# Kernel optimization log

Hardware: AMD Instinct MI355X
Metric: run time of the kernel (lower is better)

Reference implementation:

```python
import jax, jax.numpy as jnp
import numpy as np

D = 1024   # rnn_size
H = 64     # pooling MLP hidden
B, C = 16, 1024


def setup_inputs() -> dict:
    key = jax.random.key(0)
    ks = jax.random.split(key, 12)
    s = 1.0 / np.sqrt(D)
    inp = {
        "encoder_outputs": jax.random.normal(ks[0], (B, C, D), jnp.float32),
        # Linear weights stored as [in, out] (y = x @ W + b), same math as torch Linear
        "Wf": jax.random.uniform(ks[1], (D, D), jnp.float32, -s, s),
        "bf": jax.random.uniform(ks[2], (D,), jnp.float32, -s, s),
        "Wg": jax.random.uniform(ks[3], (D, D), jnp.float32, -s, s),
        "bg": jax.random.uniform(ks[4], (D,), jnp.float32, -s, s),
        "Wx": jax.random.uniform(ks[5], (D, D), jnp.float32, -s, s),
        "bx": jax.random.uniform(ks[6], (D,), jnp.float32, -s, s),
        "W1": jax.random.uniform(ks[7], (D, H), jnp.float32, -s, s),
        "b1": jax.random.uniform(ks[8], (H,), jnp.float32, -s, s),
        "W2": jax.random.uniform(ks[9], (H, 1), jnp.float32, -1.0 / np.sqrt(H), 1.0 / np.sqrt(H)),
        "b2": jax.random.uniform(ks[10], (1,), jnp.float32, -1.0 / np.sqrt(H), 1.0 / np.sqrt(H)),
        # gamma is nn.Parameter(zeros(1)); use a nonzero value for a nontrivial baseline
        "gamma": jax.random.normal(ks[11], (1,), jnp.float32) * 0.1,
    }
    return inp


def reference(encoder_outputs, Wf, bf, Wg, bg, Wx, bx, W1, b1, W2, b2, gamma):
    x = encoder_outputs                                  # [B, C, D]
    q = jax.nn.relu(x @ Wf + bf)                         # proj_query [B, C, D]
    k = jax.nn.relu(x @ Wg + bg)                         # proj_key   [B, C, D]
    v = jax.nn.relu(x @ Wx + bx)                         # proj_value [B, C, D]
    energy = jnp.einsum('bid,bjd->bij', q, k)            # [B, C, C]
    attn = jax.nn.softmax(energy, axis=1)                # softmax over dim=1 (non-standard axis)
    # out = attention^T @ v : out[b,j,d] = sum_i attn[b,i,j] * v[b,i,d]
    out = jnp.einsum('bij,bid->bjd', attn, v)            # [B, C, D]
    out = gamma * out + x                                # gamma-residual
    # MLP attention pooling over C
    e2 = jax.nn.relu(x @ W1 + b1) @ W2 + b2              # [B, C, 1]
    w = jax.nn.softmax(e2[..., 0], axis=1)               # [B, C]
    return jnp.sum(out * w[..., None], axis=1)           # [B, D]
```

## Files before the change

### kernel.cpp

```cpp
#include <hip/hip_runtime.h>

#define B_ 16
#define C_ 1024
#define D_ 1024
#define H_ 64
#define M_ (B_*C_)

typedef __attribute__((ext_vector_type(8))) short bf16x8;
typedef __attribute__((ext_vector_type(8))) unsigned short ushortx8;
typedef __attribute__((ext_vector_type(4))) float f32x4;

__device__ __forceinline__ float wave_max(float v){
  #pragma unroll
  for (int o = 32; o > 0; o >>= 1) v = fmaxf(v, __shfl_xor(v, o));
  return v;
}
__device__ __forceinline__ float wave_sum(float v){
  #pragma unroll
  for (int o = 32; o > 0; o >>= 1) v += __shfl_xor(v, o);
  return v;
}

__device__ __forceinline__ ushort f2bf(float f){
  union { float f; unsigned u; } a; a.f = f;
  unsigned r = a.u + 0x7fff + ((a.u >> 16) & 1);
  return (ushort)(r >> 16);
}
__device__ __forceinline__ float bf2f(ushort h){
  union { unsigned u; float f; } a; a.u = ((unsigned)h) << 16; return a.f;
}

__device__ __forceinline__ void lds_cp16(const ushort* g, ushort* l){
  __builtin_amdgcn_global_load_lds(
      (const __attribute__((address_space(1))) void*)g,
      (__attribute__((address_space(3))) void*)l, 16, 0, 0);
}

__global__ __launch_bounds__(256) void prep_kernel(
    const float* __restrict__ x, const float* __restrict__ Wf,
    const float* __restrict__ Wg, const float* __restrict__ Wx,
    const float* __restrict__ W1,
    ushort* __restrict__ x_bf, ushort* __restrict__ wt,
    ushort* __restrict__ w1t)
{
  __shared__ float tile[32][33];
  const int blk = blockIdx.x;
  const int t = threadIdx.x;
  if (blk < 16384) {
    const int i = blk*256 + t;
    float4 v = ((const float4*)x)[i];
    ushort4 o;
    o.x = f2bf(v.x); o.y = f2bf(v.y); o.z = f2bf(v.z); o.w = f2bf(v.w);
    ((ushort4*)x_bf)[i] = o;
  } else if (blk < 16384 + 3072) {
    const int bb = blk - 16384;
    const int z = bb >> 10, rem = bb & 1023;
    const int n0 = (rem & 31)*32, k0 = (rem >> 5)*32;
    const float* W = (z == 0) ? Wf : (z == 1) ? Wg : Wx;
    ushort* Out = wt + (size_t)z*D_*D_;
    const int tx = t & 31, ty = t >> 5;
    #pragma unroll
    for (int i = 0; i < 32; i += 8)
      tile[ty+i][tx] = W[(size_t)(k0+ty+i)*D_ + n0+tx];
    __syncthreads();
    #pragma unroll
    for (int i = 0; i < 32; i += 8)
      Out[(size_t)(n0+ty+i)*D_ + k0+tx] = f2bf(tile[tx][ty+i]);
  } else {
    const int bb = blk - 16384 - 3072;
    const int n0 = (bb & 1)*32, k0 = (bb >> 1)*32;
    const int tx = t & 31, ty = t >> 5;
    #pragma unroll
    for (int i = 0; i < 32; i += 8)
      tile[ty+i][tx] = W1[(size_t)(k0+ty+i)*H_ + n0+tx];
    __syncthreads();
    #pragma unroll
    for (int i = 0; i < 32; i += 8)
      w1t[(size_t)(n0+ty+i)*D_ + k0+tx] = f2bf(tile[tx][ty+i]);
  }
}

__global__ __launch_bounds__(256) void proj_kernel(
    const ushort* __restrict__ A, const ushort* __restrict__ Wt,
    const float* __restrict__ bf, const float* __restrict__ bg,
    const float* __restrict__ bx,
    ushort* __restrict__ q, ushort* __restrict__ k, ushort* __restrict__ v)
{
  __shared__ ushort As[128*64];
  __shared__ ushort Bs[128*64];
  const int t = threadIdx.x;
  const int wid = t >> 6, lane = t & 63;
  const int m0 = blockIdx.y * 128, n0 = blockIdx.x * 128;
  const int seg = n0 >> 10;
  const int nloc0 = n0 - (seg << 10);

  const int srow = t >> 3;
  const int sch = ((t & 7) ^ (srow & 7)) * 8;
  const ushort* gaBase = A  + (size_t)(m0 + srow)*1024 + sch;
  const ushort* gbBase = Wt + (size_t)(n0 + srow)*1024 + sch;

  const int quad = lane >> 4, l16 = lane & 15;
  const int wm = wid >> 1, wn = wid & 1;
  const int cx0 = ((0*4 + quad) ^ (l16 & 7)) * 8;
  const int cx1 = ((1*4 + quad) ^ (l16 & 7)) * 8;
  const int arow0 = (wm*64 + l16)*64;
  const int brow0 = (wn*64 + l16)*64;

  f32x4 acc[4][4] = {};

  for (int k0 = 0; k0 < 1024; k0 += 64) {
    #pragma unroll
    for (int i = 0; i < 4; ++i) {
      lds_cp16(gaBase + (size_t)(i*32)*1024, As + (8*wid + 32*i)*64);
      lds_cp16(gbBase + (size_t)(i*32)*1024, Bs + (8*wid + 32*i)*64);
    }
    gaBase += 64; gbBase += 64;
    __syncthreads();
    #pragma unroll
    for (int h = 0; h < 2; ++h) {
      const int cx = h ? cx1 : cx0;
      bf16x8 af[4], bfr[4];
      #pragma unroll
      for (int i = 0; i < 4; ++i) {
        af[i]  = *(const bf16x8*)&As[arow0 + i*1024 + cx];
        bfr[i] = *(const bf16x8*)&Bs[brow0 + i*1024 + cx];
      }
      #pragma unroll
      for (int mt = 0; mt < 4; ++mt)
        #pragma unroll
        for (int nt = 0; nt < 4; ++nt)
          acc[mt][nt] = __builtin_amdgcn_mfma_f32_16x16x32_bf16(
              af[mt], bfr[nt], acc[mt][nt], 0, 0, 0);
    }
    __syncthreads();
  }

  const float* bp = (seg == 0) ? bf : (seg == 1) ? bg : bx;
  ushort* op      = (seg == 0) ? q  : (seg == 1) ? k  : v;
  const int gm_base = m0 + wm*64 + quad*4;
  const int gn_base = nloc0 + wn*64 + l16;
  float bv[4];
  #pragma unroll
  for (int nt = 0; nt < 4; ++nt) bv[nt] = bp[gn_base + nt*16];
  #pragma unroll
  for (int mt = 0; mt < 4; ++mt)
    #pragma unroll
    for (int rr = 0; rr < 4; ++rr) {
      const size_t rowoff = (size_t)(gm_base + mt*16 + rr) * 1024;
      #pragma unroll
      for (int nt = 0; nt < 4; ++nt)
        op[rowoff + gn_base + nt*16] =
            f2bf(fmaxf(acc[mt][nt][rr] + bv[nt], 0.f));
    }
}

__global__ __launch_bounds__(256) void energy_kernel(
    const ushort* __restrict__ Km, const ushort* __restrict__ Qm,
    ushort* __restrict__ E)
{
  __shared__ ushort As[128*64];
  __shared__ ushort Bs[128*64];
  const int t = threadIdx.x;
  const int wid = t >> 6, lane = t & 63;
  const int m0 = blockIdx.y * 128, n0 = blockIdx.x * 128;
  const ushort* Ab = Km + (size_t)blockIdx.z * C_ * D_;
  const ushort* Bb = Qm + (size_t)blockIdx.z * C_ * D_;

  const int srow = t >> 3;
  const int sch = ((t & 7) ^ (srow & 7)) * 8;
  const ushort* gaBase = Ab + (size_t)(m0 + srow)*1024 + sch;
  const ushort* gbBase = Bb + (size_t)(n0 + srow)*1024 + sch;

  const int quad = lane >> 4, l16 = lane & 15;
  const int wm = wid >> 1, wn = wid & 1;
  const int cx0 = ((0*4 + quad) ^ (l16 & 7)) * 8;
  const int cx1 = ((1*4 + quad) ^ (l16 & 7)) * 8;
  const int arow0 = (wm*64 + l16)*64;
  const int brow0 = (wn*64 + l16)*64;

  f32x4 acc[4][4] = {};

  for (int k0 = 0; k0 < 1024; k0 += 64) {
    #pragma unroll
    for (int i = 0; i < 4; ++i) {
      lds_cp16(gaBase + (size_t)(i*32)*1024, As + (8*wid + 32*i)*64);
      lds_cp16(gbBase + (size_t)(i*32)*1024, Bs + (8*wid + 32*i)*64);
    }
    gaBase += 64; gbBase += 64;
    __syncthreads();
    #pragma unroll
    for (int h = 0; h < 2; ++h) {
      const int cx = h ? cx1 : cx0;
      bf16x8 af[4], bfr[4];
      #pragma unroll
      for (int i = 0; i < 4; ++i) {
        af[i]  = *(const bf16x8*)&As[arow0 + i*1024 + cx];
        bfr[i] = *(const bf16x8*)&Bs[brow0 + i*1024 + cx];
      }
      #pragma unroll
      for (int mt = 0; mt < 4; ++mt)
        #pragma unroll
        for (int nt = 0; nt < 4; ++nt)
          acc[mt][nt] = __builtin_amdgcn_mfma_f32_16x16x32_bf16(
              af[mt], bfr[nt], acc[mt][nt], 0, 0, 0);
    }
    __syncthreads();
  }

  ushort* O = E + (size_t)blockIdx.z * C_ * C_;
  const int gm_base = m0 + wm*64 + quad*4;
  const int gn_base = n0 + wn*64 + l16;
  #pragma unroll
  for (int mt = 0; mt < 4; ++mt)
    #pragma unroll
    for (int rr = 0; rr < 4; ++rr) {
      const size_t rowoff = (size_t)(gm_base + mt*16 + rr) * 1024;
      #pragma unroll
      for (int nt = 0; nt < 4; ++nt)
        O[rowoff + gn_base + nt*16] = f2bf(acc[mt][nt][rr]);
    }
}

__device__ __forceinline__ int fsw(int row){
  return (row & 3) ^ ((row >> 2) & 3);
}
__global__ __launch_bounds__(256) void pool_mfma_kernel(
    const ushort* __restrict__ A, const ushort* __restrict__ Bt,
    const float* __restrict__ b1, const float* __restrict__ W2,
    float* __restrict__ e2out)
{
  __shared__ ushort As[128*32];
  __shared__ ushort Bs[64*32];
  const int t = threadIdx.x;
  const int wid = t >> 6, lane = t & 63;
  const int m0 = blockIdx.x * 128;

  const int r = t >> 2;
  const int kc = ((t & 3) ^ fsw(r)) * 8;
  const ushort* ga0 = A + (size_t)(m0 + r)*1024 + kc;
  const ushort* ga1 = ga0 + (size_t)64*1024;
  const ushort* gb0 = Bt + (size_t)r*1024 + kc;
  ushort* lA = As + wid*512;
  ushort* lB = Bs + wid*512;

  const int quad = lane >> 4, l16 = lane & 15;
  const int fr = fsw(l16);
  const int am0 = (wid*32 + l16)*32 + ((quad ^ fr)*8);
  const int bn0 = l16*32 + ((quad ^ fr)*8);

  f32x4 acc[2][4] = {};

  for (int k0 = 0; k0 < 1024; k0 += 32) {
    lds_cp16(ga0, lA); lds_cp16(ga1, lA + 2048);
    lds_cp16(gb0, lB);
    ga0 += 32; ga1 += 32; gb0 += 32;
    __syncthreads();
    bf16x8 af[2], bfr[4];
    #pragma unroll
    for (int i = 0; i < 2; ++i) af[i] = *(const bf16x8*)&As[am0 + i*512];
    #pragma unroll
    for (int i = 0; i < 4; ++i) bfr[i] = *(const bf16x8*)&Bs[bn0 + i*512];
    #pragma unroll
    for (int mt = 0; mt < 2; ++mt)
      #pragma unroll
      for (int nt = 0; nt < 4; ++nt)
        acc[mt][nt] = __builtin_amdgcn_mfma_f32_16x16x32_bf16(
            af[mt], bfr[nt], acc[mt][nt], 0, 0, 0);
    __syncthreads();
  }

  float b1v[4], w2v[4];
  #pragma unroll
  for (int nt = 0; nt < 4; ++nt) {
    b1v[nt] = b1[nt*16 + l16];
    w2v[nt] = W2[nt*16 + l16];
  }
  #pragma unroll
  for (int mt = 0; mt < 2; ++mt)
    #pragma unroll
    for (int rr = 0; rr < 4; ++rr) {
      float h = 0.f;
      #pragma unroll
      for (int nt = 0; nt < 4; ++nt)
        h += fmaxf(acc[mt][nt][rr] + b1v[nt], 0.f) * w2v[nt];
      #pragma unroll
      for (int o = 1; o < 16; o <<= 1) h += __shfl_xor(h, o);
      if (l16 == 0)
        e2out[m0 + wid*32 + mt*16 + quad*4 + rr] = h;
    }
}

__global__ __launch_bounds__(256) void fused_sm_kernel(
    const ushort* __restrict__ E, const float* __restrict__ w,
    float* __restrict__ u_part)
{
  __shared__ float ul[4][1024];
  const int b = blockIdx.y;
  const int strip = blockIdx.x;
  const int t = threadIdx.x, wv = t >> 6, lane = t & 63;
  const ushort* Eb = E + (size_t)b*C_*C_;
  const float* wb = w + (size_t)b*C_;
  float acc[2][8] = {};
  #pragma unroll
  for (int rj = 0; rj < 4; ++rj) {
    const int j = strip*16 + wv*4 + rj;
    const ushort* row = Eb + (size_t)j*C_;
    float vv[2][8];
    float m = -1e30f;
    #pragma unroll
    for (int c = 0; c < 2; ++c) {
      ushortx8 h = *(const ushortx8*)&row[c*512 + lane*8];
      #pragma unroll
      for (int kk = 0; kk < 8; ++kk) {
        vv[c][kk] = bf2f(h[kk]);
        m = fmaxf(m, vv[c][kk]);
      }
    }
    m = wave_max(m);
    float e[2][8];
    float s = 0.f;
    #pragma unroll
    for (int c = 0; c < 2; ++c)
      #pragma unroll
      for (int kk = 0; kk < 8; ++kk) {
        e[c][kk] = expf(vv[c][kk] - m);
        s += e[c][kk];
      }
    s = wave_sum(s);
    const float sc = wb[j] / s;
    #pragma unroll
    for (int c = 0; c < 2; ++c)
      #pragma unroll
      for (int kk = 0; kk < 8; ++kk) acc[c][kk] += sc * e[c][kk];
  }
  #pragma unroll
  for (int c = 0; c < 2; ++c)
    #pragma unroll
    for (int k4 = 0; k4 < 2; ++k4) {
      float4 o;
      o.x = acc[c][k4*4+0]; o.y = acc[c][k4*4+1];
      o.z = acc[c][k4*4+2]; o.w = acc[c][k4*4+3];
      *(float4*)&ul[wv][c*512 + lane*8 + k4*4] = o;
    }
  __syncthreads();
  float4 r0 = *(float4*)&ul[0][t*4];
  float4 r1 = *(float4*)&ul[1][t*4];
  float4 r2 = *(float4*)&ul[2][t*4];
  float4 r3 = *(float4*)&ul[3][t*4];
  float4 o;
  o.x = r0.x+r1.x+r2.x+r3.x; o.y = r0.y+r1.y+r2.y+r3.y;
  o.z = r0.z+r1.z+r2.z+r3.z; o.w = r0.w+r1.w+r2.w+r3.w;
  *(float4*)&u_part[((size_t)strip*B_ + b)*C_ + t*4] = o;
}

__global__ __launch_bounds__(256) void softmax_w_kernel(
    const float* __restrict__ e2in, float* __restrict__ w)
{
  __shared__ float redm[4];
  __shared__ float reds[4];
  const int b = blockIdx.x, t = threadIdx.x;
  const int lane = t & 63, wid = t >> 6;
  const float* row = e2in + (size_t)b*C_;
  float4 v = *(const float4*)&row[t*4];
  float m = fmaxf(fmaxf(v.x, v.y), fmaxf(v.z, v.w));
  m = wave_max(m);
  if (lane == 0) redm[wid] = m;
  __syncthreads();
  m = fmaxf(fmaxf(redm[0], redm[1]), fmaxf(redm[2], redm[3]));
  float e0 = expf(v.x - m), e1 = expf(v.y - m);
  float e2 = expf(v.z - m), e3 = expf(v.w - m);
  float s = e0 + e1 + e2 + e3;
  s = wave_sum(s);
  if (lane == 0) reds[wid] = s;
  __syncthreads();
  s = reds[0] + reds[1] + reds[2] + reds[3];
  const float inv = 1.0f / s;
  float4 o; o.x = e0*inv; o.y = e1*inv; o.z = e2*inv; o.w = e3*inv;
  *(float4*)&w[(size_t)b*C_ + t*4] = o;
}

__global__ __launch_bounds__(256) void final_part_kernel(
    const ushort* __restrict__ X, const ushort* __restrict__ V,
    const float* __restrict__ u_part, const float* __restrict__ w,
    const float* __restrict__ gamma, float* __restrict__ fpart)
{
  const int b = blockIdx.x, s = blockIdx.y;
  const int t = threadIdx.x;
  __shared__ float red[16][17];
  __shared__ float us[16];
  {
    const int ii = t & 15, g = t >> 4;
    float p = 0.f;
    #pragma unroll
    for (int q2 = 0; q2 < 4; ++q2) {
      const int sp = g*4 + q2;
      p += u_part[((size_t)sp*B_ + b)*C_ + s*16 + ii];
    }
    red[ii][g] = p;
  }
  __syncthreads();
  if (t < 16) {
    float s2 = 0.f;
    #pragma unroll
    for (int g = 0; g < 16; ++g) s2 += red[t][g];
    us[t] = s2;
  }
  __syncthreads();

  const int d0 = t * 4;
  const ushort* xb = X + (size_t)b*C_*D_;
  const ushort* vb = V + (size_t)b*C_*D_;
  const float* wb = w + (size_t)b*C_;
  float4 av = {0,0,0,0}, ax = {0,0,0,0};
  #pragma unroll
  for (int ii = 0; ii < 16; ++ii) {
    const int i = s*16 + ii;
    const float ui = us[ii], wi = wb[i];
    ushort4 vv = *(const ushort4*)&vb[(size_t)i*D_ + d0];
    ushort4 xv = *(const ushort4*)&xb[(size_t)i*D_ + d0];
    av.x += ui*bf2f(vv.x); av.y += ui*bf2f(vv.y);
    av.z += ui*bf2f(vv.z); av.w += ui*bf2f(vv.w);
    ax.x += wi*bf2f(xv.x); ax.y += wi*bf2f(xv.y);
    ax.z += wi*bf2f(xv.z); ax.w += wi*bf2f(xv.w);
  }
  const float g = gamma[0];
  float4 o;
  o.x = g*av.x + ax.x; o.y = g*av.y + ax.y;
  o.z = g*av.z + ax.z; o.w = g*av.w + ax.w;
  *(float4*)&fpart[((size_t)s*B_ + b)*D_ + d0] = o;
}

__global__ __launch_bounds__(256) void final_combine_kernel(
    const float* __restrict__ fpart, float* __restrict__ out)
{
  const int idx = blockIdx.x*256 + threadIdx.x;
  float s = 0.f;
  #pragma unroll 8
  for (int sp = 0; sp < 64; ++sp) s += fpart[(size_t)sp*B_*D_ + idx];
  out[idx] = s;
}

extern "C" void kernel_launch(void* const* d_in, const int* in_sizes, int n_in,
                              void* d_out, int out_size, void* d_ws, size_t ws_size,
                              hipStream_t stream) {
  (void)in_sizes; (void)n_in; (void)out_size; (void)ws_size;
  const float* x  = (const float*)d_in[0];
  const float* Wf = (const float*)d_in[1];
  const float* bf = (const float*)d_in[2];
  const float* Wg = (const float*)d_in[3];
  const float* bg = (const float*)d_in[4];
  const float* Wx = (const float*)d_in[5];
  const float* bx = (const float*)d_in[6];
  const float* W1 = (const float*)d_in[7];
  const float* b1 = (const float*)d_in[8];
  const float* W2 = (const float*)d_in[9];
  const float* gamma = (const float*)d_in[11];
  float* out = (float*)d_out;

  ushort* x_bf = (ushort*)d_ws;
  ushort* wt   = x_bf + (size_t)M_*D_;
  ushort* w1t  = wt + (size_t)3*D_*D_;
  ushort* q_bf = w1t + (size_t)H_*D_;
  ushort* k_bf = q_bf + (size_t)M_*D_;
  ushort* v_bf = k_bf + (size_t)M_*D_;
  ushort* E    = v_bf + (size_t)M_*D_;
  float*  e2b  = (float*)(E + (size_t)B_*C_*C_);
  float*  wbuf = e2b + M_;
  float*  u_part = wbuf + M_;
  float*  fpart  = (float*)E;

  prep_kernel<<<dim3(16384+3072+64), 256, 0, stream>>>(
      x, Wf, Wg, Wx, W1, x_bf, wt, w1t);

  proj_kernel<<<dim3(24,128), 256, 0, stream>>>(x_bf, wt, bf, bg, bx,
                                                q_bf, k_bf, v_bf);

  pool_mfma_kernel<<<dim3(M_/128), 256, 0, stream>>>(x_bf, w1t, b1, W2, e2b);
  softmax_w_kernel<<<dim3(B_), 256, 0, stream>>>(e2b, wbuf);

  energy_kernel<<<dim3(8,8,B_), 256, 0, stream>>>(k_bf, q_bf, E);
  fused_sm_kernel<<<dim3(64,B_), 256, 0, stream>>>(E, wbuf, u_part);

  final_part_kernel<<<dim3(B_,64), 256, 0, stream>>>(x_bf, v_bf, u_part, wbuf,
                                                     gamma, fpart);
  final_combine_kernel<<<dim3(M_/256), 256, 0, stream>>>(fpart, out);
}
```

Measured before the change: 340.5 us.

## Remap GEMM blocks per XCD, add occupancy hints, and fold final reduction into atomics

The projection and energy GEMMs now remap their linear block IDs so that blocks sharing the same M tile land on the same XCD, which should improve L2 reuse of A tiles. Both GEMMs also get a minimum-blocks hint of 3 in launch_bounds. The final combine kernel is removed: partial sums are atomically added into the output, which prep_kernel now zeroes with 16 extra blocks. This saves one launch and the fpart round trip, at the cost of atomic contention (64 adds per output element) and a non-deterministic summation order.

```diff
diff --git a/kernel.cpp b/kernel.cpp
--- a/kernel.cpp
+++ b/kernel.cpp
@@ -41,7 +41,7 @@
     const float* __restrict__ Wg, const float* __restrict__ Wx,
     const float* __restrict__ W1,
     ushort* __restrict__ x_bf, ushort* __restrict__ wt,
-    ushort* __restrict__ w1t)
+    ushort* __restrict__ w1t, float* __restrict__ out)
 {
   __shared__ float tile[32][33];
   const int blk = blockIdx.x;
@@ -66,7 +66,7 @@
     #pragma unroll
     for (int i = 0; i < 32; i += 8)
       Out[(size_t)(n0+ty+i)*D_ + k0+tx] = f2bf(tile[tx][ty+i]);
-  } else {
+  } else if (blk < 16384 + 3072 + 64) {
     const int bb = blk - 16384 - 3072;
     const int n0 = (bb & 1)*32, k0 = (bb >> 1)*32;
     const int tx = t & 31, ty = t >> 5;
@@ -77,10 +77,14 @@
     #pragma unroll
     for (int i = 0; i < 32; i += 8)
       w1t[(size_t)(n0+ty+i)*D_ + k0+tx] = f2bf(tile[tx][ty+i]);
-  }
-}
-
-__global__ __launch_bounds__(256) void proj_kernel(
+  } else {
+    const int bb = blk - 16384 - 3072 - 64;
+    float4 z4 = {0,0,0,0};
+    ((float4*)out)[bb*256 + t] = z4;
+  }
+}
+
+__global__ __launch_bounds__(256, 3) void proj_kernel(
     const ushort* __restrict__ A, const ushort* __restrict__ Wt,
     const float* __restrict__ bf, const float* __restrict__ bg,
     const float* __restrict__ bx,
@@ -90,7 +94,13 @@
   __shared__ ushort Bs[128*64];
   const int t = threadIdx.x;
   const int wid = t >> 6, lane = t & 63;
-  const int m0 = blockIdx.y * 128, n0 = blockIdx.x * 128;
+
+  const int id = blockIdx.y * gridDim.x + blockIdx.x;
+  const int xcd = id & 7;
+  const int qq = id >> 3;
+  const int xk = qq % 24;
+  const int p  = (qq / 24) * 8 + xcd;
+  const int m0 = p * 128, n0 = xk * 128;
   const int seg = n0 >> 10;
   const int nloc0 = n0 - (seg << 10);
 
@@ -154,7 +164,7 @@
     }
 }
 
-__global__ __launch_bounds__(256) void energy_kernel(
+__global__ __launch_bounds__(256, 3) void energy_kernel(
     const ushort* __restrict__ Km, const ushort* __restrict__ Qm,
     ushort* __restrict__ E)
 {
@@ -162,9 +172,16 @@
   __shared__ ushort Bs[128*64];
   const int t = threadIdx.x;
   const int wid = t >> 6, lane = t & 63;
-  const int m0 = blockIdx.y * 128, n0 = blockIdx.x * 128;
-  const ushort* Ab = Km + (size_t)blockIdx.z * C_ * D_;
-  const ushort* Bb = Qm + (size_t)blockIdx.z * C_ * D_;
+
+  const int id = (blockIdx.z * 8 + blockIdx.y) * 8 + blockIdx.x;
+  const int xcd = id & 7;
+  const int qq = id >> 3;
+  const int xk = qq % 8;
+  const int p  = (qq / 8) * 8 + xcd;
+  const int bz = p >> 3, ym = p & 7;
+  const int m0 = ym * 128, n0 = xk * 128;
+  const ushort* Ab = Km + (size_t)bz * C_ * D_;
+  const ushort* Bb = Qm + (size_t)bz * C_ * D_;
 
   const int srow = t >> 3;
   const int sch = ((t & 7) ^ (srow & 7)) * 8;
@@ -207,7 +224,7 @@
     __syncthreads();
   }
 
-  ushort* O = E + (size_t)blockIdx.z * C_ * C_;
+  ushort* O = E + (size_t)bz * C_ * C_;
   const int gm_base = m0 + wm*64 + quad*4;
   const int gn_base = n0 + wn*64 + l16;
   #pragma unroll
@@ -382,7 +399,7 @@
 __global__ __launch_bounds__(256) void final_part_kernel(
     const ushort* __restrict__ X, const ushort* __restrict__ V,
     const float* __restrict__ u_part, const float* __restrict__ w,
-    const float* __restrict__ gamma, float* __restrict__ fpart)
+    const float* __restrict__ gamma, float* __restrict__ out)
 {
   const int b = blockIdx.x, s = blockIdx.y;
   const int t = threadIdx.x;
@@ -424,20 +441,11 @@
     ax.z += wi*bf2f(xv.z); ax.w += wi*bf2f(xv.w);
   }
   const float g = gamma[0];
-  float4 o;
-  o.x = g*av.x + ax.x; o.y = g*av.y + ax.y;
-  o.z = g*av.z + ax.z; o.w = g*av.w + ax.w;
-  *(float4*)&fpart[((size_t)s*B_ + b)*D_ + d0] = o;
-}
-
-__global__ __launch_bounds__(256) void final_combine_kernel(
-    const float* __restrict__ fpart, float* __restrict__ out)
-{
-  const int idx = blockIdx.x*256 + threadIdx.x;
-  float s = 0.f;
-  #pragma unroll 8
-  for (int sp = 0; sp < 64; ++sp) s += fpart[(size_t)sp*B_*D_ + idx];
-  out[idx] = s;
+  float* op = out + (size_t)b*D_ + d0;
+  atomicAdd(op + 0, g*av.x + ax.x);
+  atomicAdd(op + 1, g*av.y + ax.y);
+  atomicAdd(op + 2, g*av.z + ax.z);
+  atomicAdd(op + 3, g*av.w + ax.w);
 }
 
 extern "C" void kernel_launch(void* const* d_in, const int* in_sizes, int n_in,
@@ -467,10 +475,9 @@
   float*  e2b  = (float*)(E + (size_t)B_*C_*C_);
   float*  wbuf = e2b + M_;
   float*  u_part = wbuf + M_;
-  float*  fpart  = (float*)E;
-
-  prep_kernel<<<dim3(16384+3072+64), 256, 0, stream>>>(
-      x, Wf, Wg, Wx, W1, x_bf, wt, w1t);
+
+  prep_kernel<<<dim3(16384+3072+64+16), 256, 0, stream>>>(
+      x, Wf, Wg, Wx, W1, x_bf, wt, w1t, out);
 
   proj_kernel<<<dim3(24,128), 256, 0, stream>>>(x_bf, wt, bf, bg, bx,
                                                 q_bf, k_bf, v_bf);
@@ -482,6 +489,5 @@
   fused_sm_kernel<<<dim3(64,B_), 256, 0, stream>>>(E, wbuf, u_part);
 
   final_part_kernel<<<dim3(B_,64), 256, 0, stream>>>(x_bf, v_bf, u_part, wbuf,
-                                                     gamma, fpart);
-  final_combine_kernel<<<dim3(M_/256), 256, 0, stream>>>(fpart, out);
-}
+                                                     gamma, out);
+}
```

Result: no change. 342.8 us (+0.7%).
